# Kernel tuning notes

Hardware: AMD Instinct MI355X
Metric: run time of the kernel (lower is better)

## Reference

```python
import jax, jax.numpy as jnp
import numpy as np

B, T, DIM = 2, 2048, 2048
H, DH = 16, 128
QC, KVC = 512, 512
DD = 64  # decoupled rope dim


def _rope_freqs(t, dd, theta=10000.0):
    inv = 1.0 / (theta ** (np.arange(0, dd, 2, dtype=np.float32) / dd))  # [dd/2]
    ang = np.arange(t, dtype=np.float32)[:, None] * inv[None, :]         # [T, dd/2]
    return jnp.asarray(np.stack([np.cos(ang), np.sin(ang)], axis=-1))    # [T, dd/2, 2]


def setup_inputs() -> dict:
    key = jax.random.key(0)
    ks = jax.random.split(key, 10)
    def w(k, i, o):
        return jax.random.normal(k, (i, o), jnp.float32) / np.sqrt(i)
    x = jax.random.normal(ks[0], (B, T, DIM), jnp.float32)
    freqs_cis = _rope_freqs(T, DD)
    neg = jnp.float32(-1e9)
    mask = jnp.where(jnp.tril(jnp.ones((T, T), bool)), 0.0, neg).astype(jnp.float32)
    return {
        "x": x, "freqs_cis": freqs_cis, "mask": mask,
        "W_dq": w(ks[1], DIM, QC), "W_uq": w(ks[2], QC, H * DH),
        "W_dkv": w(ks[3], DIM, KVC), "W_uk": w(ks[4], KVC, H * DH),
        "W_uv": w(ks[5], KVC, H * DH), "W_qr": w(ks[6], QC, H * DD),
        "W_kr": w(ks[7], DIM, DD), "W_o": w(ks[8], H * DH, DIM),
    }


def _apply_rope(t, freqs_cis):
    # t: [B, T, H, DD]; freqs_cis: [T, DD/2, 2]
    tp = t.reshape(*t.shape[:-1], -1, 2)               # [B,T,H,DD/2,2]
    cos = freqs_cis[None, :, None, :, 0]
    sin = freqs_cis[None, :, None, :, 1]
    x1, x2 = tp[..., 0], tp[..., 1]
    rot = jnp.stack([x1 * cos - x2 * sin, x1 * sin + x2 * cos], axis=-1)
    return rot.reshape(t.shape)


def reference(x, freqs_cis, mask, W_dq, W_uq, W_dkv, W_uk, W_uv, W_qr, W_kr, W_o):
    q_c = x @ W_dq                                     # [B,T,QC]
    kv_c = x @ W_dkv                                   # [B,T,KVC]
    q_rope = (q_c @ W_qr).reshape(B, T, H, DD)
    kv_rope = jnp.broadcast_to((x @ W_kr)[:, :, None, :], (B, T, H, DD))
    q_rope = _apply_rope(q_rope, freqs_cis)
    kv_rope = _apply_rope(kv_rope, freqs_cis)
    q = (q_c @ W_uq).reshape(B, T, H, DH)
    k = (kv_c @ W_uk).reshape(B, T, H, DH)
    v = (kv_c @ W_uv).reshape(B, T, H, DH)
    q = jnp.concatenate([q, q_rope], axis=-1)          # [B,T,H,DH+DD]
    k = jnp.concatenate([k, kv_rope], axis=-1)
    scale = 1.0 / np.sqrt(DH + DD)
    scores = jnp.einsum("bqhd,bkhd->bhqk", q, k) * scale + mask[None, None]
    attn = jax.nn.softmax(scores, axis=-1)
    out = jnp.einsum("bhqk,bkhd->bqhd", attn, v).reshape(B, T, H * DH)
    return out @ W_o
```

## Files before the change

kernel.cpp:

```cpp
#include <hip/hip_runtime.h>
#include <hip/hip_bf16.h>
#include <cstdint>
#include <cstddef>

typedef __bf16 bf16_t;
typedef __attribute__((ext_vector_type(8))) __bf16 bf16x8;
typedef __attribute__((ext_vector_type(4))) __bf16 bf16x4;
typedef __attribute__((ext_vector_type(4))) float f32x4;

#define B_ 2
#define T_ 2048
#define DIM_ 2048
#define H_ 16
#define DH_ 128
#define DD_ 64
#define DQK_ 192
#define QSTRIDE_ 3072
#define BT_ 4096
#define SCALE_ 0.07216878364870322f

__device__ __forceinline__ void gload16(const void* g, void* lds) {
  __builtin_amdgcn_global_load_lds(
      (const __attribute__((address_space(1))) unsigned int*)g,
      (__attribute__((address_space(3))) unsigned int*)lds, 16, 0, 0);
}

struct bf16_4 { bf16_t a, b, c, d; };
__global__ void cast_f32_bf16(const float* __restrict__ in, bf16_t* __restrict__ out, int n4) {
  int i = blockIdx.x * blockDim.x + threadIdx.x;
  if (i >= n4) return;
  float4 v = ((const float4*)in)[i];
  bf16_4 r{(bf16_t)v.x, (bf16_t)v.y, (bf16_t)v.z, (bf16_t)v.w};
  ((bf16_4*)out)[i] = r;
}

__global__ void transpose_all(const float* __restrict__ Wdq, const float* __restrict__ Wdkv,
                              const float* __restrict__ Wkr, const float* __restrict__ Wuq,
                              const float* __restrict__ Wqr, const float* __restrict__ Wuk,
                              const float* __restrict__ Wuv, const float* __restrict__ Wo,
                              bf16_t* __restrict__ Bt1, bf16_t* __restrict__ Bt2,
                              bf16_t* __restrict__ Bt3, bf16_t* __restrict__ Wo_t) {
  __shared__ float tile[32][33];
  int id = blockIdx.x;
  const float* W; bf16_t* Wt; int K, N, Np, kt;
  if (id < 1024)      { W = Wdq;  Wt = Bt1;                          K = 2048; N = 512;  Np = 512;  kt = 64; }
  else if (id < 2048) { W = Wdkv; Wt = Bt1 + (size_t)512 * 2048;  id -= 1024; K = 2048; N = 512;  Np = 512;  kt = 64; }
  else if (id < 2304) { W = Wkr;  Wt = Bt1 + (size_t)1024 * 2048; id -= 2048; K = 2048; N = 64;   Np = 128;  kt = 64; }
  else if (id < 3328) { W = Wuq;  Wt = Bt2;                       id -= 2304; K = 512;  N = 2048; Np = 2048; kt = 16; }
  else if (id < 3840) { W = Wqr;  Wt = Bt2 + (size_t)2048 * 512;  id -= 3328; K = 512;  N = 1024; Np = 1024; kt = 16; }
  else if (id < 4864) { W = Wuk;  Wt = Bt3;                       id -= 3840; K = 512;  N = 2048; Np = 2048; kt = 16; }
  else if (id < 5888) { W = Wuv;  Wt = Bt3 + (size_t)2048 * 512;  id -= 4864; K = 512;  N = 2048; Np = 2048; kt = 16; }
  else                { W = Wo;   Wt = Wo_t;                      id -= 5888; K = 2048; N = 2048; Np = 2048; kt = 64; }
  int k0 = (id % kt) * 32, n0 = (id / kt) * 32;
  int tx = threadIdx.x, ty = threadIdx.y;
#pragma unroll
  for (int i = 0; i < 4; ++i) {
    int k = k0 + ty + i * 8, n = n0 + tx;
    float v = (k < K && n < N) ? W[(size_t)k * N + n] : 0.f;
    tile[ty + i * 8][tx] = v;
  }
  __syncthreads();
#pragma unroll
  for (int i = 0; i < 4; ++i) {
    int n = n0 + ty + i * 8, k = k0 + tx;
    if (n < Np && k < K) Wt[(size_t)n * K + k] = (bf16_t)tile[tx][ty + i * 8];
  }
}

__global__ void transpose_v(const bf16_t* __restrict__ V, bf16_t* __restrict__ Vt) {
  __shared__ bf16_t tile[64 * 64];
  int id = blockIdx.x;
  int t0 = (id & 31) * 64;
  int d0 = ((id >> 5) & 1) * 64;
  int bh = id >> 6;
  int b = bh >> 4, h = bh & 15;
  int t = threadIdx.x;
#pragma unroll
  for (int it = 0; it < 2; ++it) {
    int idx = it * 256 + t;
    int tt = idx >> 3, c = idx & 7;
    bf16x8 v = *(const bf16x8*)&V[(size_t)(b * T_ + t0 + tt) * 2048 + h * 128 + d0 + c * 8];
    int sw = (tt ^ (tt >> 3)) & 7;
    *(bf16x8*)((char*)tile + tt * 128 + 16 * (c ^ sw)) = v;
  }
  __syncthreads();
#pragma unroll
  for (int it = 0; it < 2; ++it) {
    int idx = it * 256 + t;
    int dr = idx >> 3, c = idx & 7;
    bf16_t tmp[8];
#pragma unroll
    for (int u = 0; u < 8; ++u) {
      int sw = (u ^ c) & 7;
      tmp[u] = *(const bf16_t*)((const char*)tile + (8 * c + u) * 128 + ((2 * dr) ^ (16 * sw)));
    }
    *(bf16x8*)&Vt[((size_t)bh * 128 + d0 + dr) * T_ + t0 + c * 8] = *(bf16x8*)tmp;
  }
}

template <int MODE>
__global__ __launch_bounds__(256) void gemm_bt(const bf16_t* __restrict__ A,
                                               const bf16_t* __restrict__ Bt,
                                               void* __restrict__ C0v,
                                               void* __restrict__ C1v,
                                               void* __restrict__ C2v,
                                               const float* __restrict__ fr,
                                               int M, int N, int K, int ldc) {
  __shared__ bf16_t As[128 * 32];
  __shared__ bf16_t Bs[128 * 32];
  const int t = threadIdx.x;
  const int w = t >> 6, l = t & 63, l15 = l & 15, lhi = l >> 4;
  const int m0 = blockIdx.y * 128, n0 = blockIdx.x * 128;
  const int wr = (w >> 1) * 64, wc = (w & 1) * 64;

  f32x4 zero = {0.f, 0.f, 0.f, 0.f};
  f32x4 acc[4][4];
#pragma unroll
  for (int m = 0; m < 4; ++m)
#pragma unroll
    for (int n = 0; n < 4; ++n) acc[m][n] = zero;

  const int e0 = t * 8;
  const int r0 = e0 >> 5, c0 = e0 & 31;
  const int e1 = 2048 + t * 8;
  const int r1 = e1 >> 5, c1 = e1 & 31;

  for (int k0 = 0; k0 < K; k0 += 32) {
    gload16(A + (size_t)(m0 + r0) * K + k0 + c0, &As[e0]);
    gload16(A + (size_t)(m0 + r1) * K + k0 + c1, &As[e1]);
    gload16(Bt + (size_t)(n0 + r0) * K + k0 + c0, &Bs[e0]);
    gload16(Bt + (size_t)(n0 + r1) * K + k0 + c1, &Bs[e1]);
    __syncthreads();
    bf16x8 af[4], bfr[4];
#pragma unroll
    for (int m = 0; m < 4; ++m)
      af[m] = *(const bf16x8*)&As[(wr + m * 16 + l15) * 32 + lhi * 8];
#pragma unroll
    for (int n = 0; n < 4; ++n)
      bfr[n] = *(const bf16x8*)&Bs[(wc + n * 16 + l15) * 32 + lhi * 8];
#pragma unroll
    for (int m = 0; m < 4; ++m)
#pragma unroll
      for (int n = 0; n < 4; ++n)
        acc[m][n] = __builtin_amdgcn_mfma_f32_16x16x32_bf16(af[m], bfr[n], acc[m][n], 0, 0, 0);
    __syncthreads();
  }

#pragma unroll
  for (int m = 0; m < 4; ++m) {
#pragma unroll
    for (int n = 0; n < 4; ++n) {
#pragma unroll
      for (int r = 0; r < 4; ++r) {
        int row = m0 + wr + m * 16 + lhi * 4 + r;
        int col = n0 + wc + n * 16 + l15;
        float v = acc[m][n][r];
        if (MODE == 1) {
          ((float*)C0v)[(size_t)row * ldc + col] = v;
        } else if (MODE == 3) {
          if (col < 512)       ((bf16_t*)C0v)[(size_t)row * 512 + col] = (bf16_t)v;
          else if (col < 1024) ((bf16_t*)C1v)[(size_t)row * 512 + (col - 512)] = (bf16_t)v;
          else if (col < 1088) ((bf16_t*)C2v)[(size_t)row * 64 + (col - 1024)] = (bf16_t)v;
        } else if (MODE == 4) {
          if (col < 2048) {
            ((bf16_t*)C0v)[(size_t)row * QSTRIDE_ + (col >> 7) * DQK_ + (col & 127)] =
                (bf16_t)(v * SCALE_);
          } else {
            float other = __shfl_xor(v, 1, 64);
            int tt = row & (T_ - 1);
            int j = (col & 63) >> 1;
            float2 cs = ((const float2*)fr)[tt * 32 + j];
            float o = (col & 1) ? (other * cs.y + v * cs.x) : (v * cs.x - other * cs.y);
            int hh = (col - 2048) >> 6;
            ((bf16_t*)C0v)[(size_t)row * QSTRIDE_ + hh * DQK_ + 128 + (col & 63)] =
                (bf16_t)(o * SCALE_);
          }
        } else if (MODE == 5) {
          if (col < 2048) ((bf16_t*)C0v)[(size_t)row * QSTRIDE_ + (col >> 7) * DQK_ + (col & 127)] = (bf16_t)v;
          else            ((bf16_t*)C1v)[(size_t)row * 2048 + (col - 2048)] = (bf16_t)v;
        }
      }
    }
  }
}

__global__ void rope_k(const bf16_t* __restrict__ kr, const float* __restrict__ fr,
                       bf16_t* __restrict__ Kb) {
  int idx = blockIdx.x * 256 + threadIdx.x;
  int j = idx & 31;
  int row = idx >> 5;
  int tt = row & (T_ - 1);
  float x1 = (float)kr[(size_t)row * 64 + 2 * j];
  float x2 = (float)kr[(size_t)row * 64 + 2 * j + 1];
  float c = fr[tt * 64 + 2 * j], s = fr[tt * 64 + 2 * j + 1];
  union { bf16_t h2[2]; unsigned u; } pk;
  pk.h2[0] = (bf16_t)(x1 * c - x2 * s);
  pk.h2[1] = (bf16_t)(x1 * s + x2 * c);
#pragma unroll
  for (int h = 0; h < H_; ++h) {
    *(unsigned*)&Kb[(size_t)row * QSTRIDE_ + h * DQK_ + 128 + 2 * j] = pk.u;
  }
}

#define KLDB 200
#define VLDB 72
#define PLDB 68

__global__ __launch_bounds__(256, 2) void flash_attn3(const bf16_t* __restrict__ Q,
                                                      const bf16_t* __restrict__ Kb,
                                                      const bf16_t* __restrict__ Vt,
                                                      bf16_t* __restrict__ Ob) {
  __shared__ bf16_t Ks[64 * KLDB];
  __shared__ bf16_t Vs[128 * VLDB];
  __shared__ bf16_t Ps[4][16 * PLDB];

  const int t = threadIdx.x, w = t >> 6, l = t & 63, l15 = l & 15, lhi = l >> 4;
  const int id = blockIdx.x;
  const int xcd = id & 7, sub = id >> 3;
  const int bh = xcd * 4 + (sub >> 4);
  const int qp = sub & 15;
  const int b = bh >> 4, h = bh & 15;
  const int qa = qp, qb = 31 - qp;

  int rK[6], cK[6];
#pragma unroll
  for (int i = 0; i < 6; ++i) { int idx = i * 256 + t; rK[i] = idx / 24; cK[i] = idx % 24; }
  const int rVt = t >> 3, cV = t & 7;
  const bf16_t* kbase = Kb + (size_t)b * T_ * QSTRIDE_ + h * DQK_;
  const bf16_t* vbase = Vt + (size_t)bh * DH_ * T_;

  bf16x8 kreg[6], vreg[4];
#define LOAD_TILE(K0)                                                                      \
  do {                                                                                     \
    _Pragma("unroll") for (int i = 0; i < 6; ++i)                                          \
        kreg[i] = *(const bf16x8*)(kbase + (size_t)((K0) + rK[i]) * QSTRIDE_ + cK[i] * 8); \
    _Pragma("unroll") for (int i = 0; i < 4; ++i)                                          \
        vreg[i] = *(const bf16x8*)(vbase + (size_t)(i * 32 + rVt) * T_ + (K0) + cV * 8);   \
  } while (0)
#define WRITE_TILE()                                                                       \
  do {                                                                                     \
    _Pragma("unroll") for (int i = 0; i < 6; ++i)                                          \
        *(bf16x8*)&Ks[rK[i] * KLDB + cK[i] * 8] = kreg[i];                                 \
    _Pragma("unroll") for (int i = 0; i < 4; ++i)                                          \
        *(bf16x8*)&Vs[(i * 32 + rVt) * VLDB + cV * 8] = vreg[i];                           \
  } while (0)

  f32x4 zero = {0.f, 0.f, 0.f, 0.f};

  LOAD_TILE(0);
  WRITE_TILE();
  __syncthreads();

  for (int pass = 0; pass < 2; ++pass) {
    const int qt = pass ? qb : qa;

    bf16x8 qf[6];
    {
      const bf16_t* qrow = Q + ((size_t)(b * T_ + qt * 64 + w * 16 + l15)) * QSTRIDE_ + h * DQK_;
#pragma unroll
      for (int kc = 0; kc < 6; ++kc) qf[kc] = *(const bf16x8*)(qrow + kc * 32 + lhi * 8);
    }

    float m_r[4], l_r[4];
    f32x4 accO[8];
#pragma unroll
    for (int r = 0; r < 4; ++r) { m_r[r] = -1e30f; l_r[r] = 0.f; }
#pragma unroll
    for (int n = 0; n < 8; ++n) accO[n] = zero;

    for (int kt = 0; kt <= qt; ++kt) {
      const bool last = (kt == qt);
      const bool haveNext = !(pass == 1 && last);
      if (haveNext) LOAD_TILE(last ? 0 : (kt + 1) * 64);

      f32x4 s[4];
#pragma unroll
      for (int n = 0; n < 4; ++n) s[n] = zero;
      __builtin_amdgcn_s_setprio(1);
#pragma unroll
      for (int kc = 0; kc < 6; ++kc) {
#pragma unroll
        for (int n = 0; n < 4; ++n) {
          bf16x8 kf = *(const bf16x8*)&Ks[(n * 16 + l15) * KLDB + kc * 32 + lhi * 8];
          s[n] = __builtin_amdgcn_mfma_f32_16x16x32_bf16(qf[kc], kf, s[n], 0, 0, 0);
        }
      }
      __builtin_amdgcn_s_setprio(0);

      if (last) {
#pragma unroll
        for (int n = 0; n < 4; ++n)
#pragma unroll
          for (int r = 0; r < 4; ++r) {
            int qq = w * 16 + lhi * 4 + r;
            int kk = n * 16 + l15;
            if (kk > qq) s[n][r] = -1e30f;
          }
      }
      float pmax[4];
#pragma unroll
      for (int r = 0; r < 4; ++r) {
        float v = fmaxf(fmaxf(s[0][r], s[1][r]), fmaxf(s[2][r], s[3][r]));
#pragma unroll
        for (int off = 1; off < 16; off <<= 1) v = fmaxf(v, __shfl_xor(v, off, 64));
        pmax[r] = v;
      }
      bool need = (pmax[0] > m_r[0] + 8.0f) || (pmax[1] > m_r[1] + 8.0f) ||
                  (pmax[2] > m_r[2] + 8.0f) || (pmax[3] > m_r[3] + 8.0f);
      if (__any(need ? 1 : 0)) {
        float corr[4];
#pragma unroll
        for (int r = 0; r < 4; ++r) {
          float mn = fmaxf(m_r[r], pmax[r]);
          corr[r] = __expf(m_r[r] - mn);
          m_r[r] = mn;
          l_r[r] *= corr[r];
        }
#pragma unroll
        for (int n = 0; n < 8; ++n)
#pragma unroll
          for (int r = 0; r < 4; ++r) accO[n][r] *= corr[r];
      }
      float rs[4] = {0.f, 0.f, 0.f, 0.f};
#pragma unroll
      for (int n = 0; n < 4; ++n)
#pragma unroll
        for (int r = 0; r < 4; ++r) {
          float p = __expf(s[n][r] - m_r[r]);
          rs[r] += p;
          Ps[w][(lhi * 4 + r) * PLDB + n * 16 + l15] = (bf16_t)p;
        }
#pragma unroll
      for (int r = 0; r < 4; ++r) {
        float v = rs[r];
#pragma unroll
        for (int off = 1; off < 16; off <<= 1) v += __shfl_xor(v, off, 64);
        l_r[r] += v;
      }

      __builtin_amdgcn_s_setprio(1);
#pragma unroll
      for (int kc = 0; kc < 2; ++kc) {
        bf16x4 p0 = *(const bf16x4*)&Ps[w][l15 * PLDB + kc * 32 + lhi * 8];
        bf16x4 p1 = *(const bf16x4*)&Ps[w][l15 * PLDB + kc * 32 + lhi * 8 + 4];
        bf16x8 pf = __builtin_shufflevector(p0, p1, 0, 1, 2, 3, 4, 5, 6, 7);
#pragma unroll
        for (int n = 0; n < 8; ++n) {
          bf16x8 vf = *(const bf16x8*)&Vs[(n * 16 + l15) * VLDB + kc * 32 + lhi * 8];
          accO[n] = __builtin_amdgcn_mfma_f32_16x16x32_bf16(pf, vf, accO[n], 0, 0, 0);
        }
      }
      __builtin_amdgcn_s_setprio(0);

      __syncthreads();
      if (haveNext) WRITE_TILE();
      __syncthreads();
    }

    {
      float inv[4];
#pragma unroll
      for (int r = 0; r < 4; ++r) inv[r] = 1.0f / l_r[r];
#pragma unroll
      for (int n = 0; n < 8; ++n)
#pragma unroll
        for (int r = 0; r < 4; ++r) {
          size_t row = (size_t)(b * T_ + qt * 64 + w * 16 + lhi * 4 + r);
          Ob[row * (H_ * DH_) + h * DH_ + n * 16 + l15] = (bf16_t)(accO[n][r] * inv[r]);
        }
    }
  }
#undef LOAD_TILE
#undef WRITE_TILE
}

extern "C" void kernel_launch(void* const* d_in, const int* in_sizes, int n_in,
                              void* d_out, int out_size, void* d_ws, size_t ws_size,
                              hipStream_t stream) {
  (void)in_sizes; (void)n_in; (void)out_size; (void)ws_size;
  const float* x    = (const float*)d_in[0];
  const float* fr   = (const float*)d_in[1];
  const float* Wdq  = (const float*)d_in[3];
  const float* Wuq  = (const float*)d_in[4];
  const float* Wdkv = (const float*)d_in[5];
  const float* Wuk  = (const float*)d_in[6];
  const float* Wuv  = (const float*)d_in[7];
  const float* Wqr  = (const float*)d_in[8];
  const float* Wkr  = (const float*)d_in[9];
  const float* Wo   = (const float*)d_in[10];
  float* out = (float*)d_out;

  char* ws = (char*)d_ws;
  size_t off = 0;
  auto alloc = [&](size_t bytes) -> void* {
    void* p = ws + off;
    off += (bytes + 255) & ~(size_t)255;
    return p;
  };
  bf16_t* x_bf   = (bf16_t*)alloc((size_t)BT_ * DIM_ * 2);
  bf16_t* Bt1    = (bf16_t*)alloc((size_t)1152 * 2048 * 2);
  bf16_t* Bt2    = (bf16_t*)alloc((size_t)3072 * 512 * 2);
  bf16_t* Bt3    = (bf16_t*)alloc((size_t)4096 * 512 * 2);
  bf16_t* Wo_t   = (bf16_t*)alloc((size_t)2048 * 2048 * 2);
  bf16_t* q_c    = (bf16_t*)alloc((size_t)BT_ * 512 * 2);
  bf16_t* kv_c   = (bf16_t*)alloc((size_t)BT_ * 512 * 2);
  bf16_t* k_rb   = (bf16_t*)alloc((size_t)BT_ * 64 * 2);
  bf16_t* Qbuf   = (bf16_t*)alloc((size_t)BT_ * QSTRIDE_ * 2);
  bf16_t* Kbuf   = (bf16_t*)alloc((size_t)BT_ * QSTRIDE_ * 2);
  bf16_t* Vbuf   = (bf16_t*)alloc((size_t)BT_ * 2048 * 2);
  bf16_t* Vt_g   = (bf16_t*)alloc((size_t)BT_ * 2048 * 2);
  bf16_t* AObuf  = (bf16_t*)alloc((size_t)BT_ * 2048 * 2);

  cast_f32_bf16<<<(BT_ * DIM_ / 4 + 255) / 256, 256, 0, stream>>>(x, x_bf, BT_ * DIM_ / 4);
  transpose_all<<<9984, dim3(32, 8), 0, stream>>>(Wdq, Wdkv, Wkr, Wuq, Wqr, Wuk, Wuv, Wo,
                                                  Bt1, Bt2, Bt3, Wo_t);

  gemm_bt<3><<<dim3(9, 32),  256, 0, stream>>>(x_bf, Bt1, q_c, kv_c, k_rb, nullptr, BT_, 1088, 2048, 0);
  gemm_bt<4><<<dim3(24, 32), 256, 0, stream>>>(q_c,  Bt2, Qbuf, nullptr, nullptr, fr, BT_, 3072, 512, 0);
  gemm_bt<5><<<dim3(32, 32), 256, 0, stream>>>(kv_c, Bt3, Kbuf, Vbuf, nullptr, nullptr, BT_, 4096, 512, 0);

  transpose_v<<<2048, 256, 0, stream>>>(Vbuf, Vt_g);
  rope_k<<<(BT_ * 32) / 256, 256, 0, stream>>>(k_rb, fr, Kbuf);

  flash_attn3<<<512, 256, 0, stream>>>(Qbuf, Kbuf, Vt_g, AObuf);

  gemm_bt<1><<<dim3(16, 32), 256, 0, stream>>>(AObuf, Wo_t, out, nullptr, nullptr, nullptr, BT_, 2048, 2048, 2048);
}
```

Baseline: 316.3 us.

## Widen GEMM K-step to 64 with XOR-swizzled LDS, fuse K rope, defer row-sum reduction

The GEMM now stages 64-wide K slices per barrier pair instead of 32, using an XOR swizzle on the LDS column index to avoid bank conflicts, which halves the number of sync points per tile. The key rope rotation and its broadcast to all heads move into the epilogue of the first projection GEMM, removing the separate rope_k launch and its intermediate buffer. In flash attention, the per-tile cross-lane shuffle reduction of softmax row sums is deferred to the final normalization, so each lane only accumulates partial sums inside the loop. These are three independent changes; LDS use per GEMM block doubles, which may reduce occupancy.

```diff
diff --git a/kernel.cpp b/kernel.cpp
--- a/kernel.cpp
+++ b/kernel.cpp
@@ -106,8 +106,8 @@
                                                void* __restrict__ C2v,
                                                const float* __restrict__ fr,
                                                int M, int N, int K, int ldc) {
-  __shared__ bf16_t As[128 * 32];
-  __shared__ bf16_t Bs[128 * 32];
+  __shared__ bf16_t As[128 * 64];
+  __shared__ bf16_t Bs[128 * 64];
   const int t = threadIdx.x;
   const int w = t >> 6, l = t & 63, l15 = l & 15, lhi = l >> 4;
   const int m0 = blockIdx.y * 128, n0 = blockIdx.x * 128;
@@ -120,29 +120,33 @@
 #pragma unroll
     for (int n = 0; n < 4; ++n) acc[m][n] = zero;
 
-  const int e0 = t * 8;
-  const int r0 = e0 >> 5, c0 = e0 & 31;
-  const int e1 = 2048 + t * 8;
-  const int r1 = e1 >> 5, c1 = e1 & 31;
-
-  for (int k0 = 0; k0 < K; k0 += 32) {
-    gload16(A + (size_t)(m0 + r0) * K + k0 + c0, &As[e0]);
-    gload16(A + (size_t)(m0 + r1) * K + k0 + c1, &As[e1]);
-    gload16(Bt + (size_t)(n0 + r0) * K + k0 + c0, &Bs[e0]);
-    gload16(Bt + (size_t)(n0 + r1) * K + k0 + c1, &Bs[e1]);
+  const int srow = t >> 3;
+  const int scol = (((t & 7) ^ (srow & 7)) << 3);
+  const int ldst = t * 8;
+
+  for (int k0 = 0; k0 < K; k0 += 64) {
+#pragma unroll
+    for (int j = 0; j < 4; ++j) {
+      gload16(A + (size_t)(m0 + srow + j * 32) * K + k0 + scol, &As[ldst + j * 2048]);
+      gload16(Bt + (size_t)(n0 + srow + j * 32) * K + k0 + scol, &Bs[ldst + j * 2048]);
+    }
     __syncthreads();
-    bf16x8 af[4], bfr[4];
-#pragma unroll
-    for (int m = 0; m < 4; ++m)
-      af[m] = *(const bf16x8*)&As[(wr + m * 16 + l15) * 32 + lhi * 8];
-#pragma unroll
-    for (int n = 0; n < 4; ++n)
-      bfr[n] = *(const bf16x8*)&Bs[(wc + n * 16 + l15) * 32 + lhi * 8];
-#pragma unroll
-    for (int m = 0; m < 4; ++m)
+#pragma unroll
+    for (int kk = 0; kk < 2; ++kk) {
+      const int xs = ((((kk << 2) + lhi) ^ (l15 & 7)) << 3);
+      bf16x8 af[4], bfr[4];
+#pragma unroll
+      for (int m = 0; m < 4; ++m)
+        af[m] = *(const bf16x8*)&As[(wr + m * 16 + l15) * 64 + xs];
 #pragma unroll
       for (int n = 0; n < 4; ++n)
-        acc[m][n] = __builtin_amdgcn_mfma_f32_16x16x32_bf16(af[m], bfr[n], acc[m][n], 0, 0, 0);
+        bfr[n] = *(const bf16x8*)&Bs[(wc + n * 16 + l15) * 64 + xs];
+#pragma unroll
+      for (int m = 0; m < 4; ++m)
+#pragma unroll
+        for (int n = 0; n < 4; ++n)
+          acc[m][n] = __builtin_amdgcn_mfma_f32_16x16x32_bf16(af[m], bfr[n], acc[m][n], 0, 0, 0);
+    }
     __syncthreads();
   }
 
@@ -158,9 +162,27 @@
         if (MODE == 1) {
           ((float*)C0v)[(size_t)row * ldc + col] = v;
         } else if (MODE == 3) {
-          if (col < 512)       ((bf16_t*)C0v)[(size_t)row * 512 + col] = (bf16_t)v;
-          else if (col < 1024) ((bf16_t*)C1v)[(size_t)row * 512 + (col - 512)] = (bf16_t)v;
-          else if (col < 1088) ((bf16_t*)C2v)[(size_t)row * 64 + (col - 1024)] = (bf16_t)v;
+          if (col < 512) {
+            ((bf16_t*)C0v)[(size_t)row * 512 + col] = (bf16_t)v;
+          } else if (col < 1024) {
+            ((bf16_t*)C1v)[(size_t)row * 512 + (col - 512)] = (bf16_t)v;
+          } else if (col < 1088) {
+            float other = __shfl_xor(v, 1, 64);
+            int tt = row & (T_ - 1);
+            int j = (col - 1024) >> 1;
+            float2 cs = ((const float2*)fr)[tt * 32 + j];
+            float o = (col & 1) ? (other * cs.y + v * cs.x) : (v * cs.x - other * cs.y);
+            float o2 = __shfl_xor(o, 1, 64);
+            if (!(col & 1)) {
+              union { bf16_t h2[2]; unsigned u; } pk;
+              pk.h2[0] = (bf16_t)o;
+              pk.h2[1] = (bf16_t)o2;
+              bf16_t* Kb = (bf16_t*)C2v;
+#pragma unroll
+              for (int hh = 0; hh < H_; ++hh)
+                *(unsigned*)&Kb[(size_t)row * QSTRIDE_ + hh * DQK_ + 128 + (col - 1024)] = pk.u;
+            }
+          }
         } else if (MODE == 4) {
           if (col < 2048) {
             ((bf16_t*)C0v)[(size_t)row * QSTRIDE_ + (col >> 7) * DQK_ + (col & 127)] =
@@ -184,24 +206,6 @@
   }
 }
 
-__global__ void rope_k(const bf16_t* __restrict__ kr, const float* __restrict__ fr,
-                       bf16_t* __restrict__ Kb) {
-  int idx = blockIdx.x * 256 + threadIdx.x;
-  int j = idx & 31;
-  int row = idx >> 5;
-  int tt = row & (T_ - 1);
-  float x1 = (float)kr[(size_t)row * 64 + 2 * j];
-  float x2 = (float)kr[(size_t)row * 64 + 2 * j + 1];
-  float c = fr[tt * 64 + 2 * j], s = fr[tt * 64 + 2 * j + 1];
-  union { bf16_t h2[2]; unsigned u; } pk;
-  pk.h2[0] = (bf16_t)(x1 * c - x2 * s);
-  pk.h2[1] = (bf16_t)(x1 * s + x2 * c);
-#pragma unroll
-  for (int h = 0; h < H_; ++h) {
-    *(unsigned*)&Kb[(size_t)row * QSTRIDE_ + h * DQK_ + 128 + 2 * j] = pk.u;
-  }
-}
-
 #define KLDB 200
 #define VLDB 72
 #define PLDB 68
@@ -321,22 +325,14 @@
 #pragma unroll
           for (int r = 0; r < 4; ++r) accO[n][r] *= corr[r];
       }
-      float rs[4] = {0.f, 0.f, 0.f, 0.f};
 #pragma unroll
       for (int n = 0; n < 4; ++n)
 #pragma unroll
         for (int r = 0; r < 4; ++r) {
           float p = __expf(s[n][r] - m_r[r]);
-          rs[r] += p;
+          l_r[r] += p;
           Ps[w][(lhi * 4 + r) * PLDB + n * 16 + l15] = (bf16_t)p;
         }
-#pragma unroll
-      for (int r = 0; r < 4; ++r) {
-        float v = rs[r];
-#pragma unroll
-        for (int off = 1; off < 16; off <<= 1) v += __shfl_xor(v, off, 64);
-        l_r[r] += v;
-      }
 
       __builtin_amdgcn_s_setprio(1);
 #pragma unroll
@@ -360,7 +356,12 @@
     {
       float inv[4];
 #pragma unroll
-      for (int r = 0; r < 4; ++r) inv[r] = 1.0f / l_r[r];
+      for (int r = 0; r < 4; ++r) {
+        float v = l_r[r];
+#pragma unroll
+        for (int off = 1; off < 16; off <<= 1) v += __shfl_xor(v, off, 64);
+        inv[r] = 1.0f / v;
+      }
 #pragma unroll
       for (int n = 0; n < 8; ++n)
 #pragma unroll
@@ -404,7 +405,6 @@
   bf16_t* Wo_t   = (bf16_t*)alloc((size_t)2048 * 2048 * 2);
   bf16_t* q_c    = (bf16_t*)alloc((size_t)BT_ * 512 * 2);
   bf16_t* kv_c   = (bf16_t*)alloc((size_t)BT_ * 512 * 2);
-  bf16_t* k_rb   = (bf16_t*)alloc((size_t)BT_ * 64 * 2);
   bf16_t* Qbuf   = (bf16_t*)alloc((size_t)BT_ * QSTRIDE_ * 2);
   bf16_t* Kbuf   = (bf16_t*)alloc((size_t)BT_ * QSTRIDE_ * 2);
   bf16_t* Vbuf   = (bf16_t*)alloc((size_t)BT_ * 2048 * 2);
@@ -415,12 +415,11 @@
   transpose_all<<<9984, dim3(32, 8), 0, stream>>>(Wdq, Wdkv, Wkr, Wuq, Wqr, Wuk, Wuv, Wo,
                                                   Bt1, Bt2, Bt3, Wo_t);
 
-  gemm_bt<3><<<dim3(9, 32),  256, 0, stream>>>(x_bf, Bt1, q_c, kv_c, k_rb, nullptr, BT_, 1088, 2048, 0);
+  gemm_bt<3><<<dim3(9, 32),  256, 0, stream>>>(x_bf, Bt1, q_c, kv_c, Kbuf, fr, BT_, 1088, 2048, 0);
   gemm_bt<4><<<dim3(24, 32), 256, 0, stream>>>(q_c,  Bt2, Qbuf, nullptr, nullptr, fr, BT_, 3072, 512, 0);
   gemm_bt<5><<<dim3(32, 32), 256, 0, stream>>>(kv_c, Bt3, Kbuf, Vbuf, nullptr, nullptr, BT_, 4096, 512, 0);
 
   transpose_v<<<2048, 256, 0, stream>>>(Vbuf, Vt_g);
-  rope_k<<<(BT_ * 32) / 256, 256, 0, stream>>>(k_rb, fr, Kbuf);
 
   flash_attn3<<<512, 256, 0, stream>>>(Qbuf, Kbuf, Vt_g, AObuf);
 
```

Result: faster. 294.1 us (-7.0%).
